# Optimization experiments

Measured on AMD Instinct MI355X. Metric: run time of the kernel, lower is better.

## Reference

```python
import math
import jax, jax.numpy as jnp
import numpy as np

D = 512
H = 8
HD = D // H
FF = 2048
EPS = 1e-5


def _layernorm(x, gamma, beta):
    mean = jnp.mean(x, axis=-1, keepdims=True)
    var = jnp.mean((x - mean) ** 2, axis=-1, keepdims=True)
    return gamma * (x - mean) / jnp.sqrt(var + EPS) + beta


def _attention(q, k, v, mask):
    # q,k,v: [B,H,Sq/Sk,hd]; mask: [B,Sq,Sk] additive, broadcast over heads
    scale = 1.0 / math.sqrt(q.shape[-1])
    scores = jnp.einsum('bhqd,bhkd->bhqk', q, k) * scale
    scores = scores + mask[:, None, :, :]
    probs = jax.nn.softmax(scores, axis=-1)
    return jnp.einsum('bhqk,bhkd->bhqd', probs, v)


def setup_inputs() -> dict:
    key = jax.random.key(0)
    ks = jax.random.split(key, 20)
    B, S_ENC, S_DEC = 256, 512, 64
    s = 0.02
    inp = {
        'x': jax.random.normal(ks[0], (B, S_ENC, D), jnp.float32),
        'y': jax.random.normal(ks[1], (B, S_DEC, D), jnp.float32),
        'mask': jnp.zeros((B, S_DEC, S_DEC), jnp.float32),
        'mask2': jnp.zeros((B, S_DEC, S_ENC), jnp.float32),
        # self-attention params
        'qkv_w': jax.random.normal(ks[2], (D, 3 * D), jnp.float32) * s,
        'qkv_b': jnp.zeros((3 * D,), jnp.float32),
        'sa_out_w': jax.random.normal(ks[3], (D, D), jnp.float32) * s,
        'sa_out_b': jnp.zeros((D,), jnp.float32),
        # cross-attention params
        'q_w': jax.random.normal(ks[4], (D, D), jnp.float32) * s,
        'q_b': jnp.zeros((D,), jnp.float32),
        'kv_w': jax.random.normal(ks[5], (D, 2 * D), jnp.float32) * s,
        'kv_b': jnp.zeros((2 * D,), jnp.float32),
        'ca_out_w': jax.random.normal(ks[6], (D, D), jnp.float32) * s,
        'ca_out_b': jnp.zeros((D,), jnp.float32),
        # ffn params
        'l1_w': jax.random.normal(ks[7], (D, FF), jnp.float32) * s,
        'l1_b': jnp.zeros((FF,), jnp.float32),
        'l2_w': jax.random.normal(ks[8], (FF, D), jnp.float32) * s,
        'l2_b': jnp.zeros((D,), jnp.float32),
        # layernorm params
        'g1': jnp.ones((D,), jnp.float32), 'b1': jnp.zeros((D,), jnp.float32),
        'g2': jnp.ones((D,), jnp.float32), 'b2': jnp.zeros((D,), jnp.float32),
        'g3': jnp.ones((D,), jnp.float32), 'b3': jnp.zeros((D,), jnp.float32),
    }
    return inp


def reference(x, y, mask, mask2, qkv_w, qkv_b, sa_out_w, sa_out_b,
              q_w, q_b, kv_w, kv_b, ca_out_w, ca_out_b,
              l1_w, l1_b, l2_w, l2_b, g1, b1, g2, b2, g3, b3):
    B, Sd, _ = y.shape
    Se = x.shape[1]

    # --- self attention (post-norm, dropout is identity at eval) ---
    resid = y
    qkv = y @ qkv_w + qkv_b                     # [B,Sd,3D]
    qkv = qkv.reshape(B, Sd, H, 3 * HD).transpose(0, 2, 1, 3)
    q, k, v = jnp.split(qkv, 3, axis=-1)        # each [B,H,Sd,hd]
    vals = _attention(q, k, v, mask)
    vals = vals.transpose(0, 2, 1, 3).reshape(B, Sd, D)
    y = vals @ sa_out_w + sa_out_b
    y = _layernorm(y + resid, g1, b1)

    # --- cross attention: kv from encoder x, q from decoder y ---
    resid = y
    kv = x @ kv_w + kv_b                        # [B,Se,2D]
    kv = kv.reshape(B, Se, H, 2 * HD).transpose(0, 2, 1, 3)
    k, v = jnp.split(kv, 2, axis=-1)            # each [B,H,Se,hd]
    q = (y @ q_w + q_b).reshape(B, Sd, H, HD).transpose(0, 2, 1, 3)
    vals = _attention(q, k, v, mask2)
    vals = vals.transpose(0, 2, 1, 3).reshape(B, Sd, D)
    y = vals @ ca_out_w + ca_out_b
    y = _layernorm(y + resid, g2, b2)

    # --- feed forward ---
    resid = y
    h = jax.nn.relu(y @ l1_w + l1_b)
    y = h @ l2_w + l2_b
    y = _layernorm(y + resid, g3, b3)
    return y
```

## Files before the change

kernel.cpp:

```cpp
#include <hip/hip_runtime.h>
#include <hip/hip_bf16.h>
#include <stdint.h>


#define SDEC 64
#define SENC 512
#define DMODEL 512
#define FFDIM 2048

typedef __bf16 bf16x8 __attribute__((ext_vector_type(8)));
typedef float  f32x4  __attribute__((ext_vector_type(4)));

static __device__ __forceinline__ float bf2f(unsigned short u) {
  union { unsigned int i; float f; } w; w.i = ((unsigned int)u) << 16; return w.f;
}
static __device__ __forceinline__ unsigned short f2bf(float f) {
  union { float f; unsigned int i; } w; w.f = f;
  unsigned int u = w.i;
  return (unsigned short)((u + 0x7fffu + ((u >> 16) & 1u)) >> 16);
}

static __device__ __forceinline__ void gl_lds16(const unsigned short* g, unsigned short* l) {
  __builtin_amdgcn_global_load_lds(
      (const __attribute__((address_space(1))) unsigned int*)g,
      (__attribute__((address_space(3))) unsigned int*)l,
      16, 0, 0);
}

__global__ __launch_bounds__(256)
void cvt_f32_bf16(const float* __restrict__ in, unsigned short* __restrict__ out, size_t n8)
{
  size_t i = (size_t)blockIdx.x * blockDim.x + threadIdx.x;
  const size_t stride = (size_t)gridDim.x * blockDim.x;
  for (; i < n8; i += stride) {
    const float* p = in + i * 8;
    float4 a = *(const float4*)p, b = *(const float4*)(p + 4);
    union { unsigned short s[8]; uint4 v; } u;
    u.s[0] = f2bf(a.x); u.s[1] = f2bf(a.y); u.s[2] = f2bf(a.z); u.s[3] = f2bf(a.w);
    u.s[4] = f2bf(b.x); u.s[5] = f2bf(b.y); u.s[6] = f2bf(b.z); u.s[7] = f2bf(b.w);
    *(uint4*)(out + i * 8) = u.v;
  }
}

template<int RELU>
__global__ __launch_bounds__(256, 2)
void gemm_kernel(const unsigned short* __restrict__ A, const unsigned short* __restrict__ Bt,
                 const float* __restrict__ bias, unsigned short* __restrict__ C,
                 int M, int N, int K)
{
  __shared__ unsigned short sh[4 * 128 * 32];
  const int tid = threadIdx.x;

  const int gx   = gridDim.x;
  const int nwg  = gx * gridDim.y;
  const int orig = blockIdx.y * gx + blockIdx.x;
  const int wg   = (orig & 7) * (nwg >> 3) + (orig >> 3);
  const int row0 = (wg / gx) * 128;
  const int col0 = (wg % gx) * 128;

  const int w = tid >> 6, lane = tid & 63;
  const int wm = w >> 1, wn = w & 1;
  const int gr = lane >> 2, gc = (lane & 3) * 8;

  unsigned short* As0 = sh;
  unsigned short* Bs0 = sh + 8192;

  auto STAGE = [&](int k0, int buf) {
    unsigned short* as = As0 + buf * 4096;
    unsigned short* bs = Bs0 + buf * 4096;
    #pragma unroll
    for (int i = 0; i < 2; ++i) {
      const int rbase = w * 32 + i * 16;
      gl_lds16(A  + (size_t)(row0 + rbase + gr) * K + (k0 + gc), as + rbase * 32);
      gl_lds16(Bt + (size_t)(col0 + rbase + gr) * K + (k0 + gc), bs + rbase * 32);
    }
  };

  f32x4 acc[4][4];
  #pragma unroll
  for (int i = 0; i < 4; ++i)
    #pragma unroll
    for (int j = 0; j < 4; ++j)
      acc[i][j] = (f32x4){0.f, 0.f, 0.f, 0.f};

  const int fr = lane & 15, fk = (lane >> 4) * 8;

  STAGE(0, 0);
  int cur = 0;
  for (int k0 = 0; k0 + 32 < K; k0 += 32) {
    STAGE(k0 + 32, cur ^ 1);
    asm volatile("s_waitcnt vmcnt(4)" ::: "memory");
    __builtin_amdgcn_s_barrier();
    asm volatile("" ::: "memory");
    {
      const unsigned short* as = As0 + cur * 4096;
      const unsigned short* bs = Bs0 + cur * 4096;
      bf16x8 af[4], bfr[4];
      #pragma unroll
      for (int mi = 0; mi < 4; ++mi)
        af[mi] = *(const bf16x8*)&as[(wm * 64 + mi * 16 + fr) * 32 + fk];
      #pragma unroll
      for (int ni = 0; ni < 4; ++ni)
        bfr[ni] = *(const bf16x8*)&bs[(wn * 64 + ni * 16 + fr) * 32 + fk];
      #pragma unroll
      for (int mi = 0; mi < 4; ++mi)
        #pragma unroll
        for (int ni = 0; ni < 4; ++ni)
          acc[mi][ni] = __builtin_amdgcn_mfma_f32_16x16x32_bf16(af[mi], bfr[ni], acc[mi][ni], 0, 0, 0);
    }
    asm volatile("" ::: "memory");
    __builtin_amdgcn_s_barrier();
    cur ^= 1;
  }
  asm volatile("s_waitcnt vmcnt(0)" ::: "memory");
  __builtin_amdgcn_s_barrier();
  asm volatile("" ::: "memory");
  {
    const unsigned short* as = As0 + cur * 4096;
    const unsigned short* bs = Bs0 + cur * 4096;
    bf16x8 af[4], bfr[4];
    #pragma unroll
    for (int mi = 0; mi < 4; ++mi)
      af[mi] = *(const bf16x8*)&as[(wm * 64 + mi * 16 + fr) * 32 + fk];
    #pragma unroll
    for (int ni = 0; ni < 4; ++ni)
      bfr[ni] = *(const bf16x8*)&bs[(wn * 64 + ni * 16 + fr) * 32 + fk];
    #pragma unroll
    for (int mi = 0; mi < 4; ++mi)
      #pragma unroll
      for (int ni = 0; ni < 4; ++ni)
        acc[mi][ni] = __builtin_amdgcn_mfma_f32_16x16x32_bf16(af[mi], bfr[ni], acc[mi][ni], 0, 0, 0);
  }
  asm volatile("" ::: "memory");
  __builtin_amdgcn_s_barrier();

  {
    const int fq = lane >> 4;
    #pragma unroll
    for (int ni = 0; ni < 4; ++ni) {
      const int c = wn * 64 + ni * 16 + fr;
      const float bv = bias ? bias[col0 + c] : 0.f;
      #pragma unroll
      for (int mi = 0; mi < 4; ++mi) {
        #pragma unroll
        for (int t = 0; t < 4; ++t) {
          const int r = wm * 64 + mi * 16 + fq * 4 + t;
          float v = acc[mi][ni][t] + bv;
          if (RELU) v = fmaxf(v, 0.f);
          sh[r * 128 + c] = f2bf(v);
        }
      }
    }
    __syncthreads();
    const int rr = tid >> 4;
    const int cc = (tid & 15) * 8;
    #pragma unroll
    for (int p = 0; p < 8; ++p) {
      const int r = p * 16 + rr;
      *(uint4*)(C + (size_t)(row0 + r) * N + col0 + cc) = *(const uint4*)&sh[r * 128 + cc];
    }
  }
}

__global__ __launch_bounds__(256, 2)
void attn_mfma(const unsigned short* __restrict__ qbuf, int qstride, int qmul,
               const unsigned short* __restrict__ kvbuf, int kvstride, int kmul, int kadd,
               int tokmul, int Skv, const float* __restrict__ mask,
               unsigned short* __restrict__ vals, float scale)
{
  __shared__ unsigned short Qs[64 * 72];
  __shared__ unsigned short Ks[64 * 72];
  __shared__ unsigned short Vt[64 * 72];
  __shared__ unsigned short Ps[64 * 72];

  const int nwg  = gridDim.x * gridDim.y;
  const int orig = blockIdx.y * gridDim.x + blockIdx.x;
  const int wg   = (orig & 7) * (nwg >> 3) + (orig >> 3);
  const int h = wg & 7, b = wg >> 3;

  const int tid = threadIdx.x;
  const int w = tid >> 6, lane = tid & 63;
  const int srow = tid >> 2;
  const int sc0 = (tid & 3) * 16;

  {
    const unsigned short* qg = qbuf + (size_t)(b * 64 + srow) * qstride + h * qmul + sc0;
    *(uint4*)&Qs[srow * 72 + sc0]     = *(const uint4*)qg;
    *(uint4*)&Qs[srow * 72 + sc0 + 8] = *(const uint4*)(qg + 8);
  }

  const int fr = lane & 15;
  const int fg = lane >> 4;
  const int orow = fg * 4;

  float mstate[4], lstate[4];
  f32x4 oacc[4];
  #pragma unroll
  for (int t = 0; t < 4; ++t) { mstate[t] = -1e30f; lstate[t] = 0.f; }
  #pragma unroll
  for (int ni = 0; ni < 4; ++ni) oacc[ni] = (f32x4){0.f, 0.f, 0.f, 0.f};

  for (int j0 = 0; j0 < Skv; j0 += 64) {
    __syncthreads();
    {
      const unsigned short* kg = kvbuf + (size_t)(b * tokmul + j0 + srow) * kvstride
                                 + h * kmul + kadd + sc0;
      *(uint4*)&Ks[srow * 72 + sc0]     = *(const uint4*)kg;
      *(uint4*)&Ks[srow * 72 + sc0 + 8] = *(const uint4*)(kg + 8);
      const unsigned short* vg = kg + 64;
      uint4 v0 = *(const uint4*)vg;
      uint4 v1 = *(const uint4*)(vg + 8);
      const unsigned short* vsp = (const unsigned short*)&v0;
      #pragma unroll
      for (int jj = 0; jj < 8; ++jj) Vt[(sc0 + jj) * 72 + srow] = vsp[jj];
      vsp = (const unsigned short*)&v1;
      #pragma unroll
      for (int jj = 0; jj < 8; ++jj) Vt[(sc0 + 8 + jj) * 72 + srow] = vsp[jj];
    }
    __syncthreads();

    f32x4 s[4];
    #pragma unroll
    for (int ni = 0; ni < 4; ++ni) s[ni] = (f32x4){0.f, 0.f, 0.f, 0.f};
    #pragma unroll
    for (int ks = 0; ks < 2; ++ks) {
      bf16x8 aq = *(const bf16x8*)&Qs[(w * 16 + fr) * 72 + ks * 32 + fg * 8];
      #pragma unroll
      for (int ni = 0; ni < 4; ++ni) {
        bf16x8 bk = *(const bf16x8*)&Ks[(ni * 16 + fr) * 72 + ks * 32 + fg * 8];
        s[ni] = __builtin_amdgcn_mfma_f32_16x16x32_bf16(aq, bk, s[ni], 0, 0, 0);
      }
    }

    #pragma unroll
    for (int t = 0; t < 4; ++t) {
      const int grow = w * 16 + orow + t;
      const float* mrow = mask + ((size_t)b * 64 + grow) * Skv + j0;
      float sv[4];
      float tmax = -1e30f;
      #pragma unroll
      for (int ni = 0; ni < 4; ++ni) {
        sv[ni] = s[ni][t] * scale + mrow[ni * 16 + fr];
        tmax = fmaxf(tmax, sv[ni]);
      }
      #pragma unroll
      for (int off = 1; off < 16; off <<= 1) tmax = fmaxf(tmax, __shfl_xor(tmax, off));
      const float mn = fmaxf(mstate[t], tmax);
      const float fscl = __expf(mstate[t] - mn);
      mstate[t] = mn;
      float psum = 0.f;
      #pragma unroll
      for (int ni = 0; ni < 4; ++ni) {
        float p = __expf(sv[ni] - mn);
        psum += p;
        Ps[grow * 72 + ni * 16 + fr] = f2bf(p);
      }
      #pragma unroll
      for (int off = 1; off < 16; off <<= 1) psum += __shfl_xor(psum, off);
      lstate[t] = lstate[t] * fscl + psum;
      #pragma unroll
      for (int ni = 0; ni < 4; ++ni) oacc[ni][t] *= fscl;
    }
    __syncthreads();

    #pragma unroll
    for (int ks = 0; ks < 2; ++ks) {
      bf16x8 pa = *(const bf16x8*)&Ps[(w * 16 + fr) * 72 + ks * 32 + fg * 8];
      #pragma unroll
      for (int ni = 0; ni < 4; ++ni) {
        bf16x8 vb = *(const bf16x8*)&Vt[(ni * 16 + fr) * 72 + ks * 32 + fg * 8];
        oacc[ni] = __builtin_amdgcn_mfma_f32_16x16x32_bf16(pa, vb, oacc[ni], 0, 0, 0);
      }
    }
  }

  #pragma unroll
  for (int t = 0; t < 4; ++t) {
    const int grow = w * 16 + orow + t;
    const float inv = 1.f / lstate[t];
    unsigned short* og = vals + (size_t)(b * 64 + grow) * DMODEL + h * 64;
    #pragma unroll
    for (int ni = 0; ni < 4; ++ni)
      og[ni * 16 + fr] = f2bf(oacc[ni][t] * inv);
  }
}

__global__ __launch_bounds__(256)
void ln_kernel(const unsigned short* __restrict__ proj16, const float* __restrict__ resid32,
               const unsigned short* __restrict__ resid16,
               const float* __restrict__ gamma, const float* __restrict__ beta,
               unsigned short* __restrict__ out16, float* __restrict__ out32)
{
  const int w = threadIdx.x >> 6, lane = threadIdx.x & 63;
  const size_t r = (size_t)blockIdx.x * 4 + w;
  const int d0 = lane * 8;

  float x[8];
  {
    uint4 u = *(const uint4*)(proj16 + r * DMODEL + d0);
    const unsigned short* s = (const unsigned short*)&u;
    #pragma unroll
    for (int j = 0; j < 8; ++j) x[j] = bf2f(s[j]);
  }
  if (resid32) {
    const float* p = resid32 + r * DMODEL + d0;
    float4 a = *(const float4*)p, b = *(const float4*)(p + 4);
    x[0] += a.x; x[1] += a.y; x[2] += a.z; x[3] += a.w;
    x[4] += b.x; x[5] += b.y; x[6] += b.z; x[7] += b.w;
  } else {
    uint4 u = *(const uint4*)(resid16 + r * DMODEL + d0);
    const unsigned short* s = (const unsigned short*)&u;
    #pragma unroll
    for (int j = 0; j < 8; ++j) x[j] += bf2f(s[j]);
  }

  float sum = 0.f;
  #pragma unroll
  for (int j = 0; j < 8; ++j) sum += x[j];
  #pragma unroll
  for (int off = 32; off > 0; off >>= 1) sum += __shfl_xor(sum, off);
  const float mean = sum * (1.f / DMODEL);

  float vs = 0.f;
  #pragma unroll
  for (int j = 0; j < 8; ++j) { float t = x[j] - mean; vs += t * t; }
  #pragma unroll
  for (int off = 32; off > 0; off >>= 1) vs += __shfl_xor(vs, off);
  const float rstd = rsqrtf(vs * (1.f / DMODEL) + 1e-5f);

  float4 g0 = *(const float4*)(gamma + d0), g1 = *(const float4*)(gamma + d0 + 4);
  float4 b0 = *(const float4*)(beta + d0),  b1 = *(const float4*)(beta + d0 + 4);
  const float g[8]  = {g0.x, g0.y, g0.z, g0.w, g1.x, g1.y, g1.z, g1.w};
  const float bb[8] = {b0.x, b0.y, b0.z, b0.w, b1.x, b1.y, b1.z, b1.w};
  float y[8];
  #pragma unroll
  for (int j = 0; j < 8; ++j) y[j] = g[j] * (x[j] - mean) * rstd + bb[j];

  if (out16) {
    union { unsigned short s[8]; uint4 v; } p;
    #pragma unroll
    for (int j = 0; j < 8; ++j) p.s[j] = f2bf(y[j]);
    *(uint4*)(out16 + r * DMODEL + d0) = p.v;
  }
  if (out32) {
    float* o = out32 + r * DMODEL + d0;
    *(float4*)o       = (float4){y[0], y[1], y[2], y[3]};
    *(float4*)(o + 4) = (float4){y[4], y[5], y[6], y[7]};
  }
}

__global__ __launch_bounds__(256)
void transpose_cvt(const float* __restrict__ W, unsigned short* __restrict__ Wt,
                   int K, int N)
{
  __shared__ float tile[32][33];
  const int tx = threadIdx.x, ty = threadIdx.y;
  const int n = blockIdx.x * 32 + tx;
  #pragma unroll
  for (int rr = 0; rr < 4; ++rr) {
    const int k = blockIdx.y * 32 + ty + rr * 8;
    tile[ty + rr * 8][tx] = W[(size_t)k * N + n];
  }
  __syncthreads();
  const int k2 = blockIdx.y * 32 + tx;
  #pragma unroll
  for (int rr = 0; rr < 4; ++rr) {
    const int n2 = blockIdx.x * 32 + ty + rr * 8;
    Wt[(size_t)n2 * K + k2] = f2bf(tile[tx][ty + rr * 8]);
  }
}

extern "C" void kernel_launch(void* const* d_in, const int* in_sizes, int n_in,
                              void* d_out, int out_size, void* d_ws, size_t ws_size,
                              hipStream_t stream)
{
  const float* x        = (const float*)d_in[0];
  const float* y        = (const float*)d_in[1];
  const float* mask     = (const float*)d_in[2];
  const float* mask2    = (const float*)d_in[3];
  const float* qkv_w    = (const float*)d_in[4];
  const float* qkv_b    = (const float*)d_in[5];
  const float* sa_out_w = (const float*)d_in[6];
  const float* sa_out_b = (const float*)d_in[7];
  const float* q_w      = (const float*)d_in[8];
  const float* q_b      = (const float*)d_in[9];
  const float* kv_w     = (const float*)d_in[10];
  const float* kv_b     = (const float*)d_in[11];
  const float* ca_out_w = (const float*)d_in[12];
  const float* ca_out_b = (const float*)d_in[13];
  const float* l1_w     = (const float*)d_in[14];
  const float* l1_b     = (const float*)d_in[15];
  const float* l2_w     = (const float*)d_in[16];
  const float* l2_b     = (const float*)d_in[17];
  const float* g1 = (const float*)d_in[18];
  const float* b1 = (const float*)d_in[19];
  const float* g2 = (const float*)d_in[20];
  const float* b2 = (const float*)d_in[21];
  const float* g3 = (const float*)d_in[22];
  const float* b3 = (const float*)d_in[23];

  const int B  = in_sizes[1] / (SDEC * DMODEL);
  const int M  = B * SDEC;
  const int ME = B * SENC;

  char* ws = (char*)d_ws;
  size_t off = 0;
  auto alloc = [&](size_t bytes) -> char* {
    char* p = ws + off;
    off += (bytes + 255) & ~(size_t)255;
    return p;
  };
  unsigned short* qkv_wt = (unsigned short*)alloc((size_t)1536 * 512 * 2);
  unsigned short* sa_wt  = (unsigned short*)alloc((size_t)512 * 512 * 2);
  unsigned short* q_wt   = (unsigned short*)alloc((size_t)512 * 512 * 2);
  unsigned short* kv_wt  = (unsigned short*)alloc((size_t)1024 * 512 * 2);
  unsigned short* ca_wt  = (unsigned short*)alloc((size_t)512 * 512 * 2);
  unsigned short* l1_wt  = (unsigned short*)alloc((size_t)2048 * 512 * 2);
  unsigned short* l2_wt  = (unsigned short*)alloc((size_t)512 * 2048 * 2);
  unsigned short* kvb    = (unsigned short*)alloc((size_t)ME * 1024 * 2);
  char*           xreg   = alloc((size_t)ME * 512 * 2);
  unsigned short* xb     = (unsigned short*)xreg;
  unsigned short* qkvb   = (unsigned short*)xreg;
  unsigned short* qb     = (unsigned short*)xreg;
  unsigned short* y2b    = (unsigned short*)(xreg + (size_t)16777216);
  unsigned short* valsb  = (unsigned short*)(xreg + (size_t)50331648);
  unsigned short* proj   = (unsigned short*)(xreg + (size_t)67108864);
  unsigned short* y1b    = (unsigned short*)(xreg + (size_t)100663296);
  unsigned short* yb     = (unsigned short*)(xreg + (size_t)117440512);
  unsigned short* hb     = kvb;
  (void)ws_size; (void)n_in; (void)out_size;

  dim3 tb(32, 8);
  transpose_cvt<<<dim3(1536 / 32, 512 / 32), tb, 0, stream>>>(qkv_w, qkv_wt, 512, 1536);
  transpose_cvt<<<dim3(512 / 32, 512 / 32), tb, 0, stream>>>(sa_out_w, sa_wt, 512, 512);
  transpose_cvt<<<dim3(512 / 32, 512 / 32), tb, 0, stream>>>(q_w, q_wt, 512, 512);
  transpose_cvt<<<dim3(1024 / 32, 512 / 32), tb, 0, stream>>>(kv_w, kv_wt, 512, 1024);
  transpose_cvt<<<dim3(512 / 32, 512 / 32), tb, 0, stream>>>(ca_out_w, ca_wt, 512, 512);
  transpose_cvt<<<dim3(2048 / 32, 512 / 32), tb, 0, stream>>>(l1_w, l1_wt, 512, 2048);
  transpose_cvt<<<dim3(512 / 32, 2048 / 32), tb, 0, stream>>>(l2_w, l2_wt, 2048, 512);

  const float scale = 0.125f;

  cvt_f32_bf16<<<4096, 256, 0, stream>>>(x, xb, (size_t)ME * 512 / 8);
  gemm_kernel<0><<<dim3(1024 / 128, ME / 128), 256, 0, stream>>>(xb, kv_wt, kv_b, kvb, ME, 1024, 512);

  cvt_f32_bf16<<<4096, 256, 0, stream>>>(y, yb, (size_t)M * 512 / 8);
  gemm_kernel<0><<<dim3(1536 / 128, M / 128), 256, 0, stream>>>(yb, qkv_wt, qkv_b, qkvb, M, 1536, 512);
  attn_mfma<<<dim3(8, B), 256, 0, stream>>>(qkvb, 1536, 192, qkvb, 1536, 192, 64, SDEC, SDEC, mask, valsb, scale);
  gemm_kernel<0><<<dim3(512 / 128, M / 128), 256, 0, stream>>>(valsb, sa_wt, sa_out_b, proj, M, 512, 512);
  ln_kernel<<<M / 4, 256, 0, stream>>>(proj, y, nullptr, g1, b1, y1b, nullptr);

  gemm_kernel<0><<<dim3(512 / 128, M / 128), 256, 0, stream>>>(y1b, q_wt, q_b, qb, M, 512, 512);
  attn_mfma<<<dim3(8, B), 256, 0, stream>>>(qb, 512, 64, kvb, 1024, 128, 0, SENC, SENC, mask2, valsb, scale);
  gemm_kernel<0><<<dim3(512 / 128, M / 128), 256, 0, stream>>>(valsb, ca_wt, ca_out_b, proj, M, 512, 512);
  ln_kernel<<<M / 4, 256, 0, stream>>>(proj, nullptr, y1b, g2, b2, y2b, nullptr);

  gemm_kernel<1><<<dim3(2048 / 128, M / 128), 256, 0, stream>>>(y2b, l1_wt, l1_b, hb, M, 2048, 512);
  gemm_kernel<0><<<dim3(512 / 128, M / 128), 256, 0, stream>>>(hb, l2_wt, l2_b, proj, M, 512, 2048);
  ln_kernel<<<M / 4, 256, 0, stream>>>(proj, nullptr, y2b, g3, b3, nullptr, (float*)d_out);
}
```

Measured before the change: 616.3 us.

## Triple-buffer GEMM LDS staging with XOR swizzle and MFMA priority boost

Replaces the double-buffered global-to-LDS pipeline in the GEMM kernel with a three-stage ring, so two K-tiles are in flight while one is computed. It also XOR-swizzles the 16-byte column chunk on both the staging writes and the fragment reads to cut LDS bank conflicts, and raises wave priority around the MFMA block. LDS use grows from 32 KB to 48 KB per block, which may limit the two-blocks-per-CU occupancy target. K must be at least 64.

Result: no change. 628.4 us (+2.0%).

```diff
diff --git a/kernel.cpp b/kernel.cpp
--- a/kernel.cpp
+++ b/kernel.cpp
@@ -48,7 +48,7 @@
                  const float* __restrict__ bias, unsigned short* __restrict__ C,
                  int M, int N, int K)
 {
-  __shared__ unsigned short sh[4 * 128 * 32];
+  __shared__ unsigned short sh[3 * 8192];
   const int tid = threadIdx.x;
 
   const int gx   = gridDim.x;
@@ -60,14 +60,12 @@
 
   const int w = tid >> 6, lane = tid & 63;
   const int wm = w >> 1, wn = w & 1;
-  const int gr = lane >> 2, gc = (lane & 3) * 8;
-
-  unsigned short* As0 = sh;
-  unsigned short* Bs0 = sh + 8192;
+  const int gr = lane >> 2;
+  const int gc = ((lane & 3) ^ ((lane >> 4) & 3)) * 8;
 
   auto STAGE = [&](int k0, int buf) {
-    unsigned short* as = As0 + buf * 4096;
-    unsigned short* bs = Bs0 + buf * 4096;
+    unsigned short* as = sh + buf * 8192;
+    unsigned short* bs = as + 4096;
     #pragma unroll
     for (int i = 0; i < 2; ++i) {
       const int rbase = w * 32 + i * 16;
@@ -83,54 +81,54 @@
     for (int j = 0; j < 4; ++j)
       acc[i][j] = (f32x4){0.f, 0.f, 0.f, 0.f};
 
-  const int fr = lane & 15, fk = (lane >> 4) * 8;
-
+  const int fr  = lane & 15;
+  const int fks = ((lane >> 4) ^ (fr >> 2)) * 8;
+
+  auto COMPUTE = [&](int buf) {
+    const unsigned short* as = sh + buf * 8192;
+    const unsigned short* bs = as + 4096;
+    bf16x8 af[4], bfr[4];
+    #pragma unroll
+    for (int mi = 0; mi < 4; ++mi)
+      af[mi] = *(const bf16x8*)&as[(wm * 64 + mi * 16 + fr) * 32 + fks];
+    #pragma unroll
+    for (int ni = 0; ni < 4; ++ni)
+      bfr[ni] = *(const bf16x8*)&bs[(wn * 64 + ni * 16 + fr) * 32 + fks];
+    __builtin_amdgcn_s_setprio(1);
+    #pragma unroll
+    for (int mi = 0; mi < 4; ++mi)
+      #pragma unroll
+      for (int ni = 0; ni < 4; ++ni)
+        acc[mi][ni] = __builtin_amdgcn_mfma_f32_16x16x32_bf16(af[mi], bfr[ni], acc[mi][ni], 0, 0, 0);
+    __builtin_amdgcn_s_setprio(0);
+  };
+
+  const int NT = K >> 5;
   STAGE(0, 0);
-  int cur = 0;
-  for (int k0 = 0; k0 + 32 < K; k0 += 32) {
-    STAGE(k0 + 32, cur ^ 1);
-    asm volatile("s_waitcnt vmcnt(4)" ::: "memory");
+  STAGE(32, 1);
+  int bc = 0, bn = 2;
+  for (int t = 0; t < NT - 2; ++t) {
+    STAGE((t + 2) << 5, bn);
+    asm volatile("s_waitcnt vmcnt(8)" ::: "memory");
     __builtin_amdgcn_s_barrier();
     asm volatile("" ::: "memory");
-    {
-      const unsigned short* as = As0 + cur * 4096;
-      const unsigned short* bs = Bs0 + cur * 4096;
-      bf16x8 af[4], bfr[4];
-      #pragma unroll
-      for (int mi = 0; mi < 4; ++mi)
-        af[mi] = *(const bf16x8*)&as[(wm * 64 + mi * 16 + fr) * 32 + fk];
-      #pragma unroll
-      for (int ni = 0; ni < 4; ++ni)
-        bfr[ni] = *(const bf16x8*)&bs[(wn * 64 + ni * 16 + fr) * 32 + fk];
-      #pragma unroll
-      for (int mi = 0; mi < 4; ++mi)
-        #pragma unroll
-        for (int ni = 0; ni < 4; ++ni)
-          acc[mi][ni] = __builtin_amdgcn_mfma_f32_16x16x32_bf16(af[mi], bfr[ni], acc[mi][ni], 0, 0, 0);
-    }
+    COMPUTE(bc);
     asm volatile("" ::: "memory");
     __builtin_amdgcn_s_barrier();
-    cur ^= 1;
-  }
+    bc = (bc + 1 == 3) ? 0 : bc + 1;
+    bn = (bn + 1 == 3) ? 0 : bn + 1;
+  }
+  asm volatile("s_waitcnt vmcnt(4)" ::: "memory");
+  __builtin_amdgcn_s_barrier();
+  asm volatile("" ::: "memory");
+  COMPUTE(bc);
+  asm volatile("" ::: "memory");
+  __builtin_amdgcn_s_barrier();
+  bc = (bc + 1 == 3) ? 0 : bc + 1;
   asm volatile("s_waitcnt vmcnt(0)" ::: "memory");
   __builtin_amdgcn_s_barrier();
   asm volatile("" ::: "memory");
-  {
-    const unsigned short* as = As0 + cur * 4096;
-    const unsigned short* bs = Bs0 + cur * 4096;
-    bf16x8 af[4], bfr[4];
-    #pragma unroll
-    for (int mi = 0; mi < 4; ++mi)
-      af[mi] = *(const bf16x8*)&as[(wm * 64 + mi * 16 + fr) * 32 + fk];
-    #pragma unroll
-    for (int ni = 0; ni < 4; ++ni)
-      bfr[ni] = *(const bf16x8*)&bs[(wn * 64 + ni * 16 + fr) * 32 + fk];
-    #pragma unroll
-    for (int mi = 0; mi < 4; ++mi)
-      #pragma unroll
-      for (int ni = 0; ni < 4; ++ni)
-        acc[mi][ni] = __builtin_amdgcn_mfma_f32_16x16x32_bf16(af[mi], bfr[ni], acc[mi][ni], 0, 0, 0);
-  }
+  COMPUTE(bc);
   asm volatile("" ::: "memory");
   __builtin_amdgcn_s_barrier();
 
```

## Add 256x256-tile GEMM kernel with swizzled LDS for large projections

Applied to the files above, without the earlier changes.

Adds a 512-thread GEMM using 256x256 output tiles, a K-step of 64, an XOR-swizzled LDS layout, and staging of the next tile interleaved with MFMA phases under setprio. It is used for the KV, QKV and FFN1 projections, which have large N. Each block now reuses more data per load, cutting global traffic. The existing 128-tile GEMM also gets a swizzled epilogue store to reduce LDS bank conflicts. The cost is fewer blocks (one per CU, 128KB LDS) and less latency hiding on the smaller grids.

After: 624.1 us. No clear change (+1.3%).

```diff
diff --git a/kernel.cpp b/kernel.cpp
--- a/kernel.cpp
+++ b/kernel.cpp
@@ -42,13 +42,32 @@
   }
 }
 
+#define GEMM_COMPUTE(asrc, bsrc)                                                     \
+  {                                                                                  \
+    const unsigned short* as_ = (asrc);                                              \
+    const unsigned short* bs_ = (bsrc);                                              \
+    bf16x8 af[4], bfr[4];                                                            \
+    _Pragma("unroll")                                                                \
+    for (int mi = 0; mi < 4; ++mi)                                                   \
+      af[mi] = *(const bf16x8*)&as_[(wm * 64 + mi * 16 + fr) * 32 + fk];             \
+    _Pragma("unroll")                                                                \
+    for (int ni = 0; ni < 4; ++ni)                                                   \
+      bfr[ni] = *(const bf16x8*)&bs_[(wn * 64 + ni * 16 + fr) * 32 + fk];            \
+    _Pragma("unroll")                                                                \
+    for (int mi = 0; mi < 4; ++mi)                                                   \
+      _Pragma("unroll")                                                              \
+      for (int ni = 0; ni < 4; ++ni)                                                 \
+        acc[mi][ni] = __builtin_amdgcn_mfma_f32_16x16x32_bf16(af[mi], bfr[ni],       \
+                                                              acc[mi][ni], 0, 0, 0); \
+  }
+
 template<int RELU>
 __global__ __launch_bounds__(256, 2)
 void gemm_kernel(const unsigned short* __restrict__ A, const unsigned short* __restrict__ Bt,
                  const float* __restrict__ bias, unsigned short* __restrict__ C,
                  int M, int N, int K)
 {
-  __shared__ unsigned short sh[4 * 128 * 32];
+  __shared__ unsigned short sh[2 * 8192];
   const int tid = threadIdx.x;
 
   const int gx   = gridDim.x;
@@ -62,12 +81,9 @@
   const int wm = w >> 1, wn = w & 1;
   const int gr = lane >> 2, gc = (lane & 3) * 8;
 
-  unsigned short* As0 = sh;
-  unsigned short* Bs0 = sh + 8192;
-
   auto STAGE = [&](int k0, int buf) {
-    unsigned short* as = As0 + buf * 4096;
-    unsigned short* bs = Bs0 + buf * 4096;
+    unsigned short* as = sh + buf * 8192;
+    unsigned short* bs = as + 4096;
     #pragma unroll
     for (int i = 0; i < 2; ++i) {
       const int rbase = w * 32 + i * 16;
@@ -92,22 +108,7 @@
     asm volatile("s_waitcnt vmcnt(4)" ::: "memory");
     __builtin_amdgcn_s_barrier();
     asm volatile("" ::: "memory");
-    {
-      const unsigned short* as = As0 + cur * 4096;
-      const unsigned short* bs = Bs0 + cur * 4096;
-      bf16x8 af[4], bfr[4];
-      #pragma unroll
-      for (int mi = 0; mi < 4; ++mi)
-        af[mi] = *(const bf16x8*)&as[(wm * 64 + mi * 16 + fr) * 32 + fk];
-      #pragma unroll
-      for (int ni = 0; ni < 4; ++ni)
-        bfr[ni] = *(const bf16x8*)&bs[(wn * 64 + ni * 16 + fr) * 32 + fk];
-      #pragma unroll
-      for (int mi = 0; mi < 4; ++mi)
-        #pragma unroll
-        for (int ni = 0; ni < 4; ++ni)
-          acc[mi][ni] = __builtin_amdgcn_mfma_f32_16x16x32_bf16(af[mi], bfr[ni], acc[mi][ni], 0, 0, 0);
-    }
+    GEMM_COMPUTE(sh + cur * 8192, sh + cur * 8192 + 4096);
     asm volatile("" ::: "memory");
     __builtin_amdgcn_s_barrier();
     cur ^= 1;
@@ -115,22 +116,7 @@
   asm volatile("s_waitcnt vmcnt(0)" ::: "memory");
   __builtin_amdgcn_s_barrier();
   asm volatile("" ::: "memory");
-  {
-    const unsigned short* as = As0 + cur * 4096;
-    const unsigned short* bs = Bs0 + cur * 4096;
-    bf16x8 af[4], bfr[4];
-    #pragma unroll
-    for (int mi = 0; mi < 4; ++mi)
-      af[mi] = *(const bf16x8*)&as[(wm * 64 + mi * 16 + fr) * 32 + fk];
-    #pragma unroll
-    for (int ni = 0; ni < 4; ++ni)
-      bfr[ni] = *(const bf16x8*)&bs[(wn * 64 + ni * 16 + fr) * 32 + fk];
-    #pragma unroll
-    for (int mi = 0; mi < 4; ++mi)
-      #pragma unroll
-      for (int ni = 0; ni < 4; ++ni)
-        acc[mi][ni] = __builtin_amdgcn_mfma_f32_16x16x32_bf16(af[mi], bfr[ni], acc[mi][ni], 0, 0, 0);
-  }
+  GEMM_COMPUTE(sh + cur * 8192, sh + cur * 8192 + 4096);
   asm volatile("" ::: "memory");
   __builtin_amdgcn_s_barrier();
 
@@ -147,7 +133,7 @@
           const int r = wm * 64 + mi * 16 + fq * 4 + t;
           float v = acc[mi][ni][t] + bv;
           if (RELU) v = fmaxf(v, 0.f);
-          sh[r * 128 + c] = f2bf(v);
+          sh[r * 128 + (c ^ (fq << 4))] = f2bf(v);
         }
       }
     }
@@ -157,7 +143,129 @@
     #pragma unroll
     for (int p = 0; p < 8; ++p) {
       const int r = p * 16 + rr;
-      *(uint4*)(C + (size_t)(row0 + r) * N + col0 + cc) = *(const uint4*)&sh[r * 128 + cc];
+      *(uint4*)(C + (size_t)(row0 + r) * N + col0 + cc) =
+          *(const uint4*)&sh[r * 128 + (cc ^ (w << 4))];
+    }
+  }
+}
+
+template<int RELU>
+__global__ __launch_bounds__(512, 1)
+void gemm256_kernel(const unsigned short* __restrict__ A, const unsigned short* __restrict__ Bt,
+                    const float* __restrict__ bias, unsigned short* __restrict__ C,
+                    int M, int N, int K)
+{
+  __shared__ unsigned short sh[65536];
+  const int tid = threadIdx.x;
+
+  const int gx   = gridDim.x;
+  const int nwg  = gx * gridDim.y;
+  const int orig = blockIdx.y * gx + blockIdx.x;
+  const int wg   = (orig & 7) * (nwg >> 3) + (orig >> 3);
+  const int row0 = (wg / gx) * 256;
+  const int col0 = (wg % gx) * 256;
+
+  const int w = tid >> 6, lane = tid & 63;
+  const int wm = w >> 2, wn = w & 3;
+  const int fr = lane & 15, fg = lane >> 4;
+
+  const int srl = lane >> 3;
+  const int sgc = ((lane & 7) ^ srl) * 8;
+
+  auto STAGE_PART = [&](int k0, int buf, int part) {
+    unsigned short* base = sh + buf * 32768 + ((part >= 2) ? 16384 : 0);
+    const unsigned short* G = (part >= 2) ? Bt : A;
+    const int o0 = (part >= 2) ? col0 : row0;
+    const int ph = part & 1;
+    #pragma unroll
+    for (int j = 0; j < 2; ++j) {
+      const int rt = w * 32 + ph * 16 + j * 8;
+      gl_lds16(G + (size_t)(o0 + rt + srl) * K + (k0 + sgc), base + rt * 64);
+    }
+  };
+
+  f32x4 acc[8][4];
+  #pragma unroll
+  for (int i = 0; i < 8; ++i)
+    #pragma unroll
+    for (int j = 0; j < 4; ++j)
+      acc[i][j] = (f32x4){0.f, 0.f, 0.f, 0.f};
+
+  const int NT = K >> 6;
+  #pragma unroll
+  for (int part = 0; part < 4; ++part) STAGE_PART(0, 0, part);
+
+  for (int t = 0; t < NT; ++t) {
+    const int buf = t & 1;
+    const unsigned short* as = sh + buf * 32768;
+    const unsigned short* bs = as + 16384;
+    const int kn = (t + 1) << 6;
+    asm volatile("s_waitcnt vmcnt(0)" ::: "memory");
+    __builtin_amdgcn_sched_barrier(0);
+    __builtin_amdgcn_s_barrier();
+
+    #pragma unroll
+    for (int ks = 0; ks < 2; ++ks) {
+      #pragma unroll
+      for (int mh = 0; mh < 2; ++mh) {
+        bf16x8 af[4], bfv[4];
+        #pragma unroll
+        for (int i = 0; i < 4; ++i) {
+          const int row = wm * 128 + (mh * 4 + i) * 16 + fr;
+          af[i] = *(const bf16x8*)&as[row * 64 + (((ks * 4 + fg) ^ (fr & 7)) * 8)];
+        }
+        #pragma unroll
+        for (int i = 0; i < 4; ++i) {
+          const int row = wn * 64 + i * 16 + fr;
+          bfv[i] = *(const bf16x8*)&bs[row * 64 + (((ks * 4 + fg) ^ (fr & 7)) * 8)];
+        }
+        if (t + 1 < NT) {
+          const int ph = ks * 2 + mh;
+          if (ph == 0) { STAGE_PART(kn, buf ^ 1, 0); STAGE_PART(kn, buf ^ 1, 1); }
+          if (ph == 1) { STAGE_PART(kn, buf ^ 1, 2); STAGE_PART(kn, buf ^ 1, 3); }
+        }
+        asm volatile("" ::: "memory");
+        __builtin_amdgcn_s_barrier();
+        __builtin_amdgcn_s_setprio(1);
+        #pragma unroll
+        for (int i = 0; i < 4; ++i)
+          #pragma unroll
+          for (int j = 0; j < 4; ++j)
+            acc[mh * 4 + i][j] = __builtin_amdgcn_mfma_f32_16x16x32_bf16(
+                af[i], bfv[j], acc[mh * 4 + i][j], 0, 0, 0);
+        __builtin_amdgcn_s_setprio(0);
+        asm volatile("" ::: "memory");
+        __builtin_amdgcn_s_barrier();
+      }
+    }
+  }
+
+  {
+    #pragma unroll
+    for (int j = 0; j < 4; ++j) {
+      const int c = wn * 64 + j * 16 + fr;
+      const float bv = bias ? bias[col0 + c] : 0.f;
+      const int cp = c ^ (fg << 4);
+      #pragma unroll
+      for (int i = 0; i < 8; ++i) {
+        #pragma unroll
+        for (int tt = 0; tt < 4; ++tt) {
+          const int r = wm * 128 + i * 16 + fg * 4 + tt;
+          float v = acc[i][j][tt] + bv;
+          if (RELU) v = fmaxf(v, 0.f);
+          sh[r * 256 + cp] = f2bf(v);
+        }
+      }
+    }
+    __syncthreads();
+    const int rr = tid >> 5;
+    const int cc = (tid & 31) * 8;
+    #pragma unroll
+    for (int p = 0; p < 16; ++p) {
+      const int r = p * 16 + rr;
+      const int rc = (r >> 2) & 3;
+      *(uint4*)(C + (size_t)(row0 + r) * N + col0 + cc) =
+          *(const uint4*)&sh[r * 256 + (cc ^ (rc << 4))];
     }
   }
 }
@@ -442,10 +550,10 @@
   const float scale = 0.125f;
 
   cvt_f32_bf16<<<4096, 256, 0, stream>>>(x, xb, (size_t)ME * 512 / 8);
-  gemm_kernel<0><<<dim3(1024 / 128, ME / 128), 256, 0, stream>>>(xb, kv_wt, kv_b, kvb, ME, 1024, 512);
+  gemm256_kernel<0><<<dim3(1024 / 256, ME / 256), 512, 0, stream>>>(xb, kv_wt, kv_b, kvb, ME, 1024, 512);
 
   cvt_f32_bf16<<<4096, 256, 0, stream>>>(y, yb, (size_t)M * 512 / 8);
-  gemm_kernel<0><<<dim3(1536 / 128, M / 128), 256, 0, stream>>>(yb, qkv_wt, qkv_b, qkvb, M, 1536, 512);
+  gemm256_kernel<0><<<dim3(1536 / 256, M / 256), 512, 0, stream>>>(yb, qkv_wt, qkv_b, qkvb, M, 1536, 512);
   attn_mfma<<<dim3(8, B), 256, 0, stream>>>(qkvb, 1536, 192, qkvb, 1536, 192, 64, SDEC, SDEC, mask, valsb, scale);
   gemm_kernel<0><<<dim3(512 / 128, M / 128), 256, 0, stream>>>(valsb, sa_wt, sa_out_b, proj, M, 512, 512);
   ln_kernel<<<M / 4, 256, 0, stream>>>(proj, y, nullptr, g1, b1, y1b, nullptr);
@@ -455,7 +563,7 @@
   gemm_kernel<0><<<dim3(512 / 128, M / 128), 256, 0, stream>>>(valsb, ca_wt, ca_out_b, proj, M, 512, 512);
   ln_kernel<<<M / 4, 256, 0, stream>>>(proj, nullptr, y1b, g2, b2, y2b, nullptr);
 
-  gemm_kernel<1><<<dim3(2048 / 128, M / 128), 256, 0, stream>>>(y2b, l1_wt, l1_b, hb, M, 2048, 512);
+  gemm256_kernel<1><<<dim3(2048 / 256, M / 256), 512, 0, stream>>>(y2b, l1_wt, l1_b, hb, M, 2048, 512);
   gemm_kernel<0><<<dim3(512 / 128, M / 128), 256, 0, stream>>>(hb, l2_wt, l2_b, proj, M, 512, 2048);
   ln_kernel<<<M / 4, 256, 0, stream>>>(proj, nullptr, y2b, g3, b3, nullptr, (float*)d_out);
 }
```
